# Optimization experiments

Measured on AMD Instinct MI355X. Metric: run time of the kernel, lower is better.

## Reference

```python
import jax, jax.numpy as jnp
import numpy as np

N = 10000
E = 320000
D_IN = 256
D_H = 256
D_OUT = 64
NEG_SLOPE = 0.2


def _segment_softmax(scores, seg, num_segments):
    # numerically stable softmax over variable-size neighborhoods
    m = jax.ops.segment_max(scores, seg, num_segments=num_segments)
    e = jnp.exp(scores - m[seg])
    s = jax.ops.segment_sum(e, seg, num_segments=num_segments)
    return e / s[seg]


def _gatv2_conv(x, src, dst, Wl, bl, Wr, br, att, bias):
    # PyG GATv2Conv, heads=1: lin_l on source, lin_r on target
    xl = x @ Wl + bl              # [N, C]
    xr = x @ Wr + br              # [N, C]
    xj = xl[src]                  # [E, C] source messages
    e = jax.nn.leaky_relu(xj + xr[dst], NEG_SLOPE)   # [E, C]
    score = e @ att               # [E]
    alpha = _segment_softmax(score, dst, N)          # [E]
    out = jax.ops.segment_sum(alpha[:, None] * xj, dst, num_segments=N)
    return out + bias


def setup_inputs() -> dict:
    key = jax.random.key(0)
    ks = jax.random.split(key, 16)
    s1 = 1.0 / np.sqrt(D_IN)
    s2 = 1.0 / np.sqrt(D_H)
    x = jax.random.normal(ks[0], (N, D_IN), dtype=jnp.float32)
    edge_index = jax.random.randint(ks[1], (2, E), 0, N, dtype=jnp.int64)
    return {
        "x": x,
        "W1l": jax.random.normal(ks[2], (D_IN, D_H), jnp.float32) * s1,
        "b1l": jnp.zeros((D_H,), jnp.float32),
        "W1r": jax.random.normal(ks[3], (D_IN, D_H), jnp.float32) * s1,
        "b1r": jnp.zeros((D_H,), jnp.float32),
        "att1": jax.random.normal(ks[4], (D_H,), jnp.float32) * s2,
        "bias1": jnp.zeros((D_H,), jnp.float32),
        "W2l": jax.random.normal(ks[5], (D_H, D_H), jnp.float32) * s2,
        "b2l": jnp.zeros((D_H,), jnp.float32),
        "W2r": jax.random.normal(ks[6], (D_H, D_H), jnp.float32) * s2,
        "b2r": jnp.zeros((D_H,), jnp.float32),
        "att2": jax.random.normal(ks[7], (D_H,), jnp.float32) * s2,
        "bias2": jnp.zeros((D_H,), jnp.float32),
        "Wout": jax.random.normal(ks[8], (D_H, D_OUT), jnp.float32) * s2,
        "bout": jnp.zeros((D_OUT,), jnp.float32),
        "edge_index": edge_index,
    }


def reference(x, W1l, b1l, W1r, b1r, att1, bias1,
              W2l, b2l, W2r, b2r, att2, bias2,
              Wout, bout, edge_index):
    # add self loops (PyG GATv2Conv default)
    loops = jnp.arange(N, dtype=edge_index.dtype)
    src = jnp.concatenate([edge_index[0], loops])
    dst = jnp.concatenate([edge_index[1], loops])

    h = _gatv2_conv(x, src, dst, W1l, b1l, W1r, b1r, att1, bias1)
    h = jax.nn.relu(h)            # norm=Identity, dropout inactive (eval)
    h = _gatv2_conv(h, src, dst, W2l, b2l, W2r, b2r, att2, bias2)
    h = jax.nn.relu(h)
    logits = h @ Wout + bout      # [N, D_OUT]
    return jax.nn.log_softmax(logits, axis=1)
```

## Files before the change

### kernel.cpp

```cpp
#include <hip/hip_runtime.h>
#include <hip/hip_bf16.h>
#include <math.h>

#define N_NODES 10000
#define N_EDGES 320000
#define TOT_E (N_EDGES + N_NODES)
#define D 256
#define DOUT 64
#define NEG_SLOPE 0.2f
#define MAXDEG 128

typedef __attribute__((ext_vector_type(8))) short bf16x8;
typedef __attribute__((ext_vector_type(4))) float f32x4;
typedef unsigned short ushort_t;

__device__ __forceinline__ unsigned short f2b_rne(float f) {
    unsigned int x = __float_as_uint(f);
    x += 0x7FFFu + ((x >> 16) & 1u);
    return (unsigned short)(x >> 16);
}
__device__ __forceinline__ float b2f(unsigned short h) {
    return __uint_as_float(((unsigned int)h) << 16);
}
__device__ __forceinline__ void bsplit(float v, unsigned short& hi, unsigned short& lo) {
    hi = f2b_rne(v);
    lo = f2b_rne(v - b2f(hi));
}

__device__ __forceinline__ void gload16(const ushort_t* g, ushort_t* l) {
    __builtin_amdgcn_global_load_lds(
        (const __attribute__((address_space(1))) void*)g,
        (__attribute__((address_space(3))) void*)l, 16, 0, 0);
}

__device__ __forceinline__ bool detect_f32(const void* x) {
    const ushort_t* xb = (const ushort_t*)x;
    int lane = threadIdx.x & 63;
    int bad = 0;
    #pragma unroll
    for (int i = 0; i < 4; ++i) {
        float v = b2f(xb[2 * (lane + 64 * i)]);
        bad += !(fabsf(v) < 1e4f) ? 1 : 0;
    }
    #pragma unroll
    for (int o = 32; o > 0; o >>= 1) bad += __shfl_down(bad, o);
    return __shfl(bad, 0) > 8;
}
__device__ __forceinline__ bool detect_i64(const int* e32) {
    int lane = threadIdx.x & 63;
    int nz = (e32[2 * lane + 1] != 0) ? 1 : 0;
    #pragma unroll
    for (int o = 32; o > 0; o >>= 1) nz += __shfl_down(nz, o);
    return __shfl(nz, 0) == 0;
}

__global__ __launch_bounds__(256) void prep_kernel(
        const void* x, ushort_t* xh, ushort_t* xlo,
        const void* W1l, const void* W1r, const void* W2l, const void* W2r, const void* Wo,
        const void* v0, const void* v1, const void* v2, const void* v3,
        const void* v4, const void* v5, const void* v6, const void* v7, const void* v8,
        ushort_t* wt, float* vecf, int* counts) {
    bool f32s = detect_f32(x);
    int bid = blockIdx.x;
    int t = threadIdx.x;
    if (bid < 2500) {
        int i = bid * 1024 + t * 4;
        float v[4];
        if (f32s) {
            float4 f = *(const float4*)((const float*)x + i);
            v[0] = f.x; v[1] = f.y; v[2] = f.z; v[3] = f.w;
        } else {
            union { uint2 q; ushort_t u[4]; } r;
            r.q = *(const uint2*)((const ushort_t*)x + i);
            #pragma unroll
            for (int j = 0; j < 4; ++j) v[j] = b2f(r.u[j]);
        }
        union { uint2 q; ushort_t u[4]; } H, L;
        #pragma unroll
        for (int j = 0; j < 4; ++j) bsplit(v[j], H.u[j], L.u[j]);
        *(uint2*)(xh + i) = H.q;
        *(uint2*)(xlo + i) = L.q;
    } else if (bid < 3588) {
        int b = bid - 2500;
        const void* srcs5[5] = {W1l, W1r, W2l, W2r, Wo};
        int wid, n, ncols;
        if (b < 1024) { wid = b >> 8; n = b & 255; ncols = 256; }
        else          { wid = 4;      n = b - 1024; ncols = 64; }
        ushort_t* dh;
        ushort_t* dl;
        if (wid < 4) { dh = wt + (size_t)wid * 2 * 65536; dl = dh + 65536; }
        else         { dh = wt + (size_t)8 * 65536;       dl = dh + 16384; }
        float v = f32s ? ((const float*)srcs5[wid])[(size_t)t * ncols + n]
                       : b2f(((const ushort_t*)srcs5[wid])[(size_t)t * ncols + n]);
        unsigned short hi, lo;
        bsplit(v, hi, lo);
        dh[(size_t)n * 256 + t] = hi;
        dl[(size_t)n * 256 + t] = lo;
    } else if (bid < 3597) {
        int b = bid - 3588;
        const void* ps[9] = {v0, v1, v2, v3, v4, v5, v6, v7, v8};
        int n = (b == 8) ? DOUT : 256;
        if (t < n) {
            float v = f32s ? ((const float*)ps[b])[t] : b2f(((const ushort_t*)ps[b])[t]);
            vecf[b * 256 + t] = v;
        }
    } else {
        int idx = (bid - 3597) * 256 + t;
        if (idx < N_NODES) counts[idx] = 0;
    }
}

__device__ __forceinline__ int eload(const int* ei, bool is64, int idx) {
    int v = is64 ? ei[2 * (size_t)idx] : ei[idx];
    return ((unsigned)v < (unsigned)N_NODES) ? v : 0;
}

__global__ __launch_bounds__(256, 3) void gemm_mfma_kernel(
        const ushort_t* __restrict__ Ahg, const ushort_t* __restrict__ Alg,
        const ushort_t* __restrict__ Wh0, const ushort_t* __restrict__ Wl0,
        const float* __restrict__ bias0, ushort_t* __restrict__ out0,
        const ushort_t* __restrict__ Wh1, const ushort_t* __restrict__ Wl1,
        const float* __restrict__ bias1, ushort_t* __restrict__ out1,
        const int* __restrict__ ei, int* __restrict__ counts,
        int* __restrict__ srcs_pad) {
    __shared__ __align__(16) ushort_t AhL[2][4096];
    __shared__ __align__(16) ushort_t AlL[2][4096];
    __shared__ __align__(16) ushort_t BhL[2][2048];
    __shared__ __align__(16) ushort_t BlL[2][2048];
    int tid = threadIdx.x;
    int lane = tid & 63, wave = tid >> 6;

    if (blockIdx.y >= 79) {
        bool is64 = detect_i64(ei);
        int id = ((blockIdx.y - 79) * 8 + blockIdx.x) * 256 + tid;
        if (id < TOT_E) {
            int src, dst;
            if (id < N_EDGES) { src = eload(ei, is64, id); dst = eload(ei, is64, N_EDGES + id); }
            else              { src = dst = id - N_EDGES; }
            int slot = atomicAdd(&counts[dst], 1);
            if (slot < MAXDEG) srcs_pad[dst * MAXDEG + slot] = src;
        }
        return;
    }

    int lin = blockIdx.x + 8 * blockIdx.y;
    int v = (lin & 7) * 79 + (lin >> 3);
    int row0 = (v >> 3) * 128;
    int y = v & 7;
    const ushort_t* Wh; const ushort_t* Wl; const float* bias;
    ushort_t* outp;
    int col0;
    if (y < 4) { Wh = Wh0; Wl = Wl0; bias = bias0; col0 = y * 64; outp = out0; }
    else       { Wh = Wh1; Wl = Wl1; bias = bias1; col0 = (y - 4) * 64; outp = out1; }

    const ushort_t* gp[6];
    ushort_t* lp0[6];
    ushort_t* lp1[6];
    {
        int lane4 = lane >> 2;
        int qsl = (lane & 3) ^ (lane4 & 3);
        #pragma unroll
        for (int j = 0; j < 6; ++j) {
            int q = wave * 6 + j;
            if (q < 8) {
                gp[j] = Ahg + (size_t)(row0 + q * 16 + lane4) * 256 + qsl * 8;
                lp0[j] = &AhL[0][q * 512]; lp1[j] = &AhL[1][q * 512];
            } else if (q < 16) {
                int r = q - 8;
                gp[j] = Alg + (size_t)(row0 + r * 16 + lane4) * 256 + qsl * 8;
                lp0[j] = &AlL[0][r * 512]; lp1[j] = &AlL[1][r * 512];
            } else if (q < 20) {
                int r = q - 16;
                gp[j] = Wh + (size_t)(col0 + r * 16 + lane4) * 256 + qsl * 8;
                lp0[j] = &BhL[0][r * 512]; lp1[j] = &BhL[1][r * 512];
            } else {
                int r = q - 20;
                gp[j] = Wl + (size_t)(col0 + r * 16 + lane4) * 256 + qsl * 8;
                lp0[j] = &BlL[0][r * 512]; lp1[j] = &BlL[1][r * 512];
            }
        }
    }
    int wm = wave >> 1, wn = wave & 1;
    int l15 = lane & 15;
    int slot = (lane >> 4) ^ (lane & 3);

    f32x4 acc[4][2];
    #pragma unroll
    for (int mg = 0; mg < 4; ++mg)
        #pragma unroll
        for (int ng = 0; ng < 2; ++ng) acc[mg][ng] = (f32x4){0.f, 0.f, 0.f, 0.f};

    #pragma unroll
    for (int j = 0; j < 6; ++j) { gload16(gp[j], lp0[j]); gp[j] += 32; }
    __syncthreads();

    #pragma unroll
    for (int s = 0; s < 8; ++s) {
        const int cb = s & 1;
        if (s < 7) {
            #pragma unroll
            for (int j = 0; j < 6; ++j) {
                gload16(gp[j], cb ? lp0[j] : lp1[j]);
                gp[j] += 32;
            }
        }
        bf16x8 ah[4], al[4];
        #pragma unroll
        for (int mg = 0; mg < 4; ++mg) {
            int o = (wm * 64 + mg * 16 + l15) * 32 + slot * 8;
            ah[mg] = *(const bf16x8*)&AhL[cb][o];
            al[mg] = *(const bf16x8*)&AlL[cb][o];
        }
        #pragma unroll
        for (int ng = 0; ng < 2; ++ng) {
            int o = (wn * 32 + ng * 16 + l15) * 32 + slot * 8;
            bf16x8 b_h = *(const bf16x8*)&BhL[cb][o];
            bf16x8 b_l = *(const bf16x8*)&BlL[cb][o];
            #pragma unroll
            for (int mg = 0; mg < 4; ++mg) {
                acc[mg][ng] = __builtin_amdgcn_mfma_f32_16x16x32_bf16(ah[mg], b_l, acc[mg][ng], 0, 0, 0);
                acc[mg][ng] = __builtin_amdgcn_mfma_f32_16x16x32_bf16(al[mg], b_h, acc[mg][ng], 0, 0, 0);
                acc[mg][ng] = __builtin_amdgcn_mfma_f32_16x16x32_bf16(ah[mg], b_h, acc[mg][ng], 0, 0, 0);
            }
        }
        __syncthreads();
    }

    int quad = lane >> 4;
    #pragma unroll
    for (int ng = 0; ng < 2; ++ng) {
        int col = col0 + wn * 32 + ng * 16 + l15;
        float bv = bias[col];
        #pragma unroll
        for (int mg = 0; mg < 4; ++mg) {
            #pragma unroll
            for (int i = 0; i < 4; ++i) {
                int row = row0 + wm * 64 + mg * 16 + quad * 4 + i;
                if (row < N_NODES) {
                    float vv = acc[mg][ng][i] + bv;
                    outp[(size_t)row * D + col] = f2b_rne(vv);
                }
            }
        }
    }
}

__global__ __launch_bounds__(256) void conv_kernel(const ushort_t* __restrict__ xl,
                                                   const ushort_t* __restrict__ xrb,
                                                   const float* __restrict__ att,
                                                   const float* __restrict__ bias,
                                                   const int* __restrict__ counts,
                                                   const int* __restrict__ srcs_pad,
                                                   ushort_t* __restrict__ hh,
                                                   ushort_t* __restrict__ hl) {
    __shared__ float fbuf[8][256];
    __shared__ float sred[8];
    int node = blockIdx.x;
    int t = threadIdx.x;
    int lane = t & 63;
    int hw = t >> 5;
    int seg = t & 31;
    int deg = counts[node];
    if (deg > MAXDEG) deg = MAXDEG;
    if (deg <= 0) {
        float o = fmaxf(bias[t], 0.f);
        unsigned short hi, lo; bsplit(o, hi, lo);
        hh[(size_t)node * D + t] = hi;
        hl[(size_t)node * D + t] = lo;
        return;
    }
    int s0 = srcs_pad[node * MAXDEG + lane];
    int s1 = srcs_pad[node * MAXDEG + 64 + lane];
    float xr8[8], att8[8];
    {
        union { uint4 q; ushort_t u[8]; } rr;
        rr.q = *(const uint4*)(xrb + (size_t)node * D + seg * 8);
        float4 a0 = *(const float4*)(att + seg * 8);
        float4 a1 = *(const float4*)(att + seg * 8 + 4);
        #pragma unroll
        for (int j = 0; j < 8; ++j) xr8[j] = b2f(rr.u[j]);
        att8[0] = a0.x; att8[1] = a0.y; att8[2] = a0.z; att8[3] = a0.w;
        att8[4] = a1.x; att8[5] = a1.y; att8[6] = a1.z; att8[7] = a1.w;
    }
    float acc8[8];
    #pragma unroll
    for (int j = 0; j < 8; ++j) acc8[j] = 0.f;
    float s = 0.f;

    for (int e0 = 0; e0 < deg; e0 += 32) {
        int dlim = deg - e0; if (dlim > 32) dlim = 32;
        int ni = (dlim > hw) ? ((dlim - hw + 7) >> 3) : 0;
        union { uint4 q; ushort_t u[8]; } r[4];
        #pragma unroll
        for (int i = 0; i < 4; ++i) {
            if (i < ni) {
                int e = e0 + hw + 8 * i;
                int src = __shfl((e < 64) ? s0 : s1, e & 63);
                r[i].q = *(const uint4*)(xl + (size_t)src * D + seg * 8);
            }
        }
        #pragma unroll
        for (int i = 0; i < 4; ++i) {
            if (i < ni) {
                float xf[8];
                #pragma unroll
                for (int j = 0; j < 8; ++j) xf[j] = b2f(r[i].u[j]);
                float p = 0.f;
                #pragma unroll
                for (int j = 0; j < 8; ++j) {
                    float v = xf[j] + xr8[j];
                    v = fmaxf(v, NEG_SLOPE * v);
                    p = fmaf(v, att8[j], p);
                }
                #pragma unroll
                for (int o = 16; o > 0; o >>= 1) p += __shfl_xor(p, o, 32);
                p = __expf(fminf(fmaxf(p, -80.f), 80.f));
                s += p;
                #pragma unroll
                for (int j = 0; j < 8; ++j) acc8[j] = fmaf(p, xf[j], acc8[j]);
            }
        }
    }
    *(float4*)&fbuf[hw][seg * 8] = (float4){acc8[0], acc8[1], acc8[2], acc8[3]};
    *(float4*)&fbuf[hw][seg * 8 + 4] = (float4){acc8[4], acc8[5], acc8[6], acc8[7]};
    if (seg == 0) sred[hw] = s;
    __syncthreads();
    float tot = 0.f;
    #pragma unroll
    for (int k = 0; k < 8; ++k) tot += fbuf[k][t];
    float stot = sred[0];
    #pragma unroll
    for (int k = 1; k < 8; ++k) stot += sred[k];
    float o = tot / stot + bias[t];
    if (!isfinite(o)) o = 0.f;
    o = fmaxf(o, 0.f);
    unsigned short hi, lo; bsplit(o, hi, lo);
    hh[(size_t)node * D + t] = hi;
    hl[(size_t)node * D + t] = lo;
}

__global__ __launch_bounds__(256) void logits_kernel(
        const ushort_t* __restrict__ Ahg, const ushort_t* __restrict__ Alg,
        const ushort_t* __restrict__ Wh, const ushort_t* __restrict__ Wl,
        const float* __restrict__ bias, float* __restrict__ out) {
    __shared__ bf16x8 Ah[4][64];
    __shared__ bf16x8 Al[4][64];
    __shared__ bf16x8 Bh[4][64];
    __shared__ bf16x8 Bl[4][64];
    __shared__ float Cs[64][65];
    __shared__ float mxs[64], lss[64];
    int tid = threadIdx.x;
    int lane = tid & 63, wave = tid >> 6;
    int row0 = blockIdx.x * 64;
    int sm = tid >> 2, skq = tid & 3;
    int sl = skq * 16 + (sm & 15), sr = sm >> 4;

    f32x4 acc[4];
    #pragma unroll
    for (int c = 0; c < 4; ++c) acc[c] = (f32x4){0.f, 0.f, 0.f, 0.f};

    for (int k0 = 0; k0 < D; k0 += 32) {
        uint4 qah, qal;
        int grow = row0 + sm;
        if (grow < N_NODES) {
            size_t aoff = (size_t)grow * D + k0 + skq * 8;
            qah = *(const uint4*)(Ahg + aoff);
            qal = *(const uint4*)(Alg + aoff);
        } else {
            qah = (uint4){0, 0, 0, 0}; qal = (uint4){0, 0, 0, 0};
        }
        size_t boff = (size_t)sm * 256 + k0 + skq * 8;
        uint4 qbh = *(const uint4*)(Wh + boff);
        uint4 qbl = *(const uint4*)(Wl + boff);
        __syncthreads();
        *(uint4*)&Ah[sr][sl] = qah;
        *(uint4*)&Al[sr][sl] = qal;
        *(uint4*)&Bh[sr][sl] = qbh;
        *(uint4*)&Bl[sr][sl] = qbl;
        __syncthreads();
        bf16x8 a_h = Ah[wave][lane];
        bf16x8 a_l = Al[wave][lane];
        #pragma unroll
        for (int c = 0; c < 4; ++c) {
            bf16x8 b_h = Bh[c][lane];
            bf16x8 b_l = Bl[c][lane];
            acc[c] = __builtin_amdgcn_mfma_f32_16x16x32_bf16(a_h, b_l, acc[c], 0, 0, 0);
            acc[c] = __builtin_amdgcn_mfma_f32_16x16x32_bf16(a_l, b_h, acc[c], 0, 0, 0);
            acc[c] = __builtin_amdgcn_mfma_f32_16x16x32_bf16(a_h, b_h, acc[c], 0, 0, 0);
        }
    }
    int quad = lane >> 4;
    #pragma unroll
    for (int c = 0; c < 4; ++c) {
        int col = c * 16 + (lane & 15);
        float bv = bias[col];
        #pragma unroll
        for (int i = 0; i < 4; ++i) {
            int row = wave * 16 + quad * 4 + i;
            Cs[row][col] = acc[c][i] + bv;
        }
    }
    __syncthreads();
    if (tid < 64) {
        float mx = -INFINITY;
        for (int c2 = 0; c2 < 64; ++c2) {
            float v = Cs[tid][c2];
            if (!isfinite(v)) { v = -1e30f; Cs[tid][c2] = v; }
            mx = fmaxf(mx, v);
        }
        float ssum = 0.f;
        for (int c2 = 0; c2 < 64; ++c2) ssum += expf(Cs[tid][c2] - mx);
        mxs[tid] = mx;
        lss[tid] = logf(ssum);
    }
    __syncthreads();
    for (int idx = tid; idx < 64 * 64; idx += 256) {
        int r = idx >> 6, col = idx & 63;
        int grow = row0 + r;
        if (grow < N_NODES) out[(size_t)grow * DOUT + col] = Cs[r][col] - mxs[r] - lss[r];
    }
}

extern "C" void kernel_launch(void* const* d_in, const int* in_sizes, int n_in,
                              void* d_out, int out_size, void* d_ws, size_t ws_size,
                              hipStream_t stream) {
    const void* x    = d_in[0];
    const void* W1l  = d_in[1];
    const void* b1l  = d_in[2];
    const void* W1r  = d_in[3];
    const void* b1r  = d_in[4];
    const void* att1 = d_in[5];
    const void* bia1 = d_in[6];
    const void* W2l  = d_in[7];
    const void* b2l  = d_in[8];
    const void* W2r  = d_in[9];
    const void* b2r  = d_in[10];
    const void* att2 = d_in[11];
    const void* bia2 = d_in[12];
    const void* Wout = d_in[13];
    const void* bout = d_in[14];
    const int*  ei   = (const int*)d_in[15];

    int* counts   = (int*)d_ws;
    int* srcs_pad = counts + N_NODES;
    ushort_t* wt = (ushort_t*)(srcs_pad + (size_t)N_NODES * MAXDEG);
    ushort_t* W1lH = wt;                ushort_t* W1lL = W1lH + 65536;
    ushort_t* W1rH = W1lL + 65536;      ushort_t* W1rL = W1rH + 65536;
    ushort_t* W2lH = W1rL + 65536;      ushort_t* W2lL = W2lH + 65536;
    ushort_t* W2rH = W2lL + 65536;      ushort_t* W2rL = W2rH + 65536;
    ushort_t* WoH  = W2rL + 65536;      ushort_t* WoL  = WoH + 16384;
    float* vecf = (float*)(WoL + 16384);
    ushort_t* xh  = (ushort_t*)(vecf + 9 * 256);
    ushort_t* xlo = xh + (size_t)N_NODES * D;
    ushort_t* xlb = xlo + (size_t)N_NODES * D;
    ushort_t* xrb = xlb + (size_t)N_NODES * D;
    ushort_t* hh = xh;
    ushort_t* hl = xlo;

    float* b1lf = vecf + 0 * 256;
    float* b1rf = vecf + 1 * 256;
    float* att1f = vecf + 2 * 256;
    float* bia1f = vecf + 3 * 256;
    float* b2lf = vecf + 4 * 256;
    float* b2rf = vecf + 5 * 256;
    float* att2f = vecf + 6 * 256;
    float* bia2f = vecf + 7 * 256;
    float* boutf = vecf + 8 * 256;

    prep_kernel<<<3637, 256, 0, stream>>>(x, xh, xlo,
                                          W1l, W1r, W2l, W2r, Wout,
                                          b1l, b1r, att1, bia1, b2l, b2r, att2, bia2, bout,
                                          wt, vecf, counts);

    gemm_mfma_kernel<<<dim3(8, 79 + 162), 256, 0, stream>>>(
        xh, xlo, W1lH, W1lL, b1lf, xlb, W1rH, W1rL, b1rf, xrb,
        ei, counts, srcs_pad);
    conv_kernel<<<N_NODES, 256, 0, stream>>>(xlb, xrb, att1f, bia1f,
                                             counts, srcs_pad, hh, hl);
    gemm_mfma_kernel<<<dim3(8, 79), 256, 0, stream>>>(
        hh, hl, W2lH, W2lL, b2lf, xlb, W2rH, W2rL, b2rf, xrb,
        nullptr, nullptr, nullptr);
    conv_kernel<<<N_NODES, 256, 0, stream>>>(xlb, xrb, att2f, bia2f,
                                             counts, srcs_pad, hh, hl);
    logits_kernel<<<(N_NODES + 63) / 64, 256, 0, stream>>>(hh, hl, WoH, WoL, boutf, (float*)d_out);
}
```

Before: 218.7 us.

## Fuse all stages into one persistent cooperative kernel with grid syncs

Replaces the six separate launches (prep, two GEMMs, two conv passes, logits) with one persistent cooperative mega-kernel. Blocks loop over virtual block indices in each phase, and grid.sync barriers with thread fences sit between phases. This removes launch overhead and inter-kernel gaps, but the grid is capped at occupancy times 256 blocks (at most 768), so each phase runs fewer concurrent blocks. It also adds grid-wide barrier costs and may lower occupancy because of the larger shared memory footprint.

Result: slower. 818.8 us (+274.3%).

```diff
diff --git a/kernel.cpp b/kernel.cpp
--- a/kernel.cpp
+++ b/kernel.cpp
@@ -1,6 +1,9 @@
 #include <hip/hip_runtime.h>
+#include <hip/hip_cooperative_groups.h>
 #include <hip/hip_bf16.h>
 #include <math.h>
+
+namespace cg = cooperative_groups;
 
 #define N_NODES 10000
 #define N_EDGES 320000
@@ -53,97 +56,37 @@
     for (int o = 32; o > 0; o >>= 1) nz += __shfl_down(nz, o);
     return __shfl(nz, 0) == 0;
 }
-
-__global__ __launch_bounds__(256) void prep_kernel(
-        const void* x, ushort_t* xh, ushort_t* xlo,
-        const void* W1l, const void* W1r, const void* W2l, const void* W2r, const void* Wo,
-        const void* v0, const void* v1, const void* v2, const void* v3,
-        const void* v4, const void* v5, const void* v6, const void* v7, const void* v8,
-        ushort_t* wt, float* vecf, int* counts) {
-    bool f32s = detect_f32(x);
-    int bid = blockIdx.x;
-    int t = threadIdx.x;
-    if (bid < 2500) {
-        int i = bid * 1024 + t * 4;
-        float v[4];
-        if (f32s) {
-            float4 f = *(const float4*)((const float*)x + i);
-            v[0] = f.x; v[1] = f.y; v[2] = f.z; v[3] = f.w;
-        } else {
-            union { uint2 q; ushort_t u[4]; } r;
-            r.q = *(const uint2*)((const ushort_t*)x + i);
-            #pragma unroll
-            for (int j = 0; j < 4; ++j) v[j] = b2f(r.u[j]);
-        }
-        union { uint2 q; ushort_t u[4]; } H, L;
-        #pragma unroll
-        for (int j = 0; j < 4; ++j) bsplit(v[j], H.u[j], L.u[j]);
-        *(uint2*)(xh + i) = H.q;
-        *(uint2*)(xlo + i) = L.q;
-    } else if (bid < 3588) {
-        int b = bid - 2500;
-        const void* srcs5[5] = {W1l, W1r, W2l, W2r, Wo};
-        int wid, n, ncols;
-        if (b < 1024) { wid = b >> 8; n = b & 255; ncols = 256; }
-        else          { wid = 4;      n = b - 1024; ncols = 64; }
-        ushort_t* dh;
-        ushort_t* dl;
-        if (wid < 4) { dh = wt + (size_t)wid * 2 * 65536; dl = dh + 65536; }
-        else         { dh = wt + (size_t)8 * 65536;       dl = dh + 16384; }
-        float v = f32s ? ((const float*)srcs5[wid])[(size_t)t * ncols + n]
-                       : b2f(((const ushort_t*)srcs5[wid])[(size_t)t * ncols + n]);
-        unsigned short hi, lo;
-        bsplit(v, hi, lo);
-        dh[(size_t)n * 256 + t] = hi;
-        dl[(size_t)n * 256 + t] = lo;
-    } else if (bid < 3597) {
-        int b = bid - 3588;
-        const void* ps[9] = {v0, v1, v2, v3, v4, v5, v6, v7, v8};
-        int n = (b == 8) ? DOUT : 256;
-        if (t < n) {
-            float v = f32s ? ((const float*)ps[b])[t] : b2f(((const ushort_t*)ps[b])[t]);
-            vecf[b * 256 + t] = v;
-        }
-    } else {
-        int idx = (bid - 3597) * 256 + t;
-        if (idx < N_NODES) counts[idx] = 0;
-    }
-}
-
 __device__ __forceinline__ int eload(const int* ei, bool is64, int idx) {
     int v = is64 ? ei[2 * (size_t)idx] : ei[idx];
     return ((unsigned)v < (unsigned)N_NODES) ? v : 0;
 }
 
-__global__ __launch_bounds__(256, 3) void gemm_mfma_kernel(
-        const ushort_t* __restrict__ Ahg, const ushort_t* __restrict__ Alg,
-        const ushort_t* __restrict__ Wh0, const ushort_t* __restrict__ Wl0,
-        const float* __restrict__ bias0, ushort_t* __restrict__ out0,
-        const ushort_t* __restrict__ Wh1, const ushort_t* __restrict__ Wl1,
-        const float* __restrict__ bias1, ushort_t* __restrict__ out1,
-        const int* __restrict__ ei, int* __restrict__ counts,
-        int* __restrict__ srcs_pad) {
-    __shared__ __align__(16) ushort_t AhL[2][4096];
-    __shared__ __align__(16) ushort_t AlL[2][4096];
-    __shared__ __align__(16) ushort_t BhL[2][2048];
-    __shared__ __align__(16) ushort_t BlL[2][2048];
+struct MegaP {
+    const void* x;
+    const void* W1l; const void* b1l; const void* W1r; const void* b1r;
+    const void* att1; const void* bia1;
+    const void* W2l; const void* b2l; const void* W2r; const void* b2r;
+    const void* att2; const void* bia2;
+    const void* Wout; const void* bout;
+    const int* ei;
+    int* counts; int* srcs_pad;
+    ushort_t* wt; float* vecf;
+    ushort_t* xh; ushort_t* xlo; ushort_t* xlb; ushort_t* xrb;
+    float* out;
+};
+
+__device__ void gemm_tile(unsigned char* SM, int lin,
+                          const ushort_t* Ahg, const ushort_t* Alg,
+                          const ushort_t* Wh0, const ushort_t* Wl0,
+                          const float* bias0, ushort_t* out0,
+                          const ushort_t* Wh1, const ushort_t* Wl1,
+                          const float* bias1, ushort_t* out1) {
+    ushort_t* AhL = (ushort_t*)SM;
+    ushort_t* AlL = AhL + 8192;
+    ushort_t* BhL = AlL + 8192;
+    ushort_t* BlL = BhL + 4096;
     int tid = threadIdx.x;
     int lane = tid & 63, wave = tid >> 6;
-
-    if (blockIdx.y >= 79) {
-        bool is64 = detect_i64(ei);
-        int id = ((blockIdx.y - 79) * 8 + blockIdx.x) * 256 + tid;
-        if (id < TOT_E) {
-            int src, dst;
-            if (id < N_EDGES) { src = eload(ei, is64, id); dst = eload(ei, is64, N_EDGES + id); }
-            else              { src = dst = id - N_EDGES; }
-            int slot = atomicAdd(&counts[dst], 1);
-            if (slot < MAXDEG) srcs_pad[dst * MAXDEG + slot] = src;
-        }
-        return;
-    }
-
-    int lin = blockIdx.x + 8 * blockIdx.y;
     int v = (lin & 7) * 79 + (lin >> 3);
     int row0 = (v >> 3) * 128;
     int y = v & 7;
@@ -164,19 +107,19 @@
             int q = wave * 6 + j;
             if (q < 8) {
                 gp[j] = Ahg + (size_t)(row0 + q * 16 + lane4) * 256 + qsl * 8;
-                lp0[j] = &AhL[0][q * 512]; lp1[j] = &AhL[1][q * 512];
+                lp0[j] = AhL + q * 512; lp1[j] = AhL + 4096 + q * 512;
             } else if (q < 16) {
                 int r = q - 8;
                 gp[j] = Alg + (size_t)(row0 + r * 16 + lane4) * 256 + qsl * 8;
-                lp0[j] = &AlL[0][r * 512]; lp1[j] = &AlL[1][r * 512];
+                lp0[j] = AlL + r * 512; lp1[j] = AlL + 4096 + r * 512;
             } else if (q < 20) {
                 int r = q - 16;
                 gp[j] = Wh + (size_t)(col0 + r * 16 + lane4) * 256 + qsl * 8;
-                lp0[j] = &BhL[0][r * 512]; lp1[j] = &BhL[1][r * 512];
+                lp0[j] = BhL + r * 512; lp1[j] = BhL + 2048 + r * 512;
             } else {
                 int r = q - 20;
                 gp[j] = Wl + (size_t)(col0 + r * 16 + lane4) * 256 + qsl * 8;
-                lp0[j] = &BlL[0][r * 512]; lp1[j] = &BlL[1][r * 512];
+                lp0[j] = BlL + r * 512; lp1[j] = BlL + 2048 + r * 512;
             }
         }
     }
@@ -208,14 +151,14 @@
         #pragma unroll
         for (int mg = 0; mg < 4; ++mg) {
             int o = (wm * 64 + mg * 16 + l15) * 32 + slot * 8;
-            ah[mg] = *(const bf16x8*)&AhL[cb][o];
-            al[mg] = *(const bf16x8*)&AlL[cb][o];
+            ah[mg] = *(const bf16x8*)&AhL[cb * 4096 + o];
+            al[mg] = *(const bf16x8*)&AlL[cb * 4096 + o];
         }
         #pragma unroll
         for (int ng = 0; ng < 2; ++ng) {
             int o = (wn * 32 + ng * 16 + l15) * 32 + slot * 8;
-            bf16x8 b_h = *(const bf16x8*)&BhL[cb][o];
-            bf16x8 b_l = *(const bf16x8*)&BlL[cb][o];
+            bf16x8 b_h = *(const bf16x8*)&BhL[cb * 2048 + o];
+            bf16x8 b_l = *(const bf16x8*)&BlL[cb * 2048 + o];
             #pragma unroll
             for (int mg = 0; mg < 4; ++mg) {
                 acc[mg][ng] = __builtin_amdgcn_mfma_f32_16x16x32_bf16(ah[mg], b_l, acc[mg][ng], 0, 0, 0);
@@ -245,242 +188,330 @@
     }
 }
 
-__global__ __launch_bounds__(256) void conv_kernel(const ushort_t* __restrict__ xl,
-                                                   const ushort_t* __restrict__ xrb,
-                                                   const float* __restrict__ att,
-                                                   const float* __restrict__ bias,
-                                                   const int* __restrict__ counts,
-                                                   const int* __restrict__ srcs_pad,
-                                                   ushort_t* __restrict__ hh,
-                                                   ushort_t* __restrict__ hl) {
-    __shared__ float fbuf[8][256];
-    __shared__ float sred[8];
-    int node = blockIdx.x;
-    int t = threadIdx.x;
-    int lane = t & 63;
-    int hw = t >> 5;
-    int seg = t & 31;
-    int deg = counts[node];
-    if (deg > MAXDEG) deg = MAXDEG;
-    if (deg <= 0) {
-        float o = fmaxf(bias[t], 0.f);
-        unsigned short hi, lo; bsplit(o, hi, lo);
-        hh[(size_t)node * D + t] = hi;
-        hl[(size_t)node * D + t] = lo;
-        return;
-    }
-    int s0 = srcs_pad[node * MAXDEG + lane];
-    int s1 = srcs_pad[node * MAXDEG + 64 + lane];
-    float xr8[8], att8[8];
-    {
-        union { uint4 q; ushort_t u[8]; } rr;
-        rr.q = *(const uint4*)(xrb + (size_t)node * D + seg * 8);
-        float4 a0 = *(const float4*)(att + seg * 8);
-        float4 a1 = *(const float4*)(att + seg * 8 + 4);
-        #pragma unroll
-        for (int j = 0; j < 8; ++j) xr8[j] = b2f(rr.u[j]);
-        att8[0] = a0.x; att8[1] = a0.y; att8[2] = a0.z; att8[3] = a0.w;
-        att8[4] = a1.x; att8[5] = a1.y; att8[6] = a1.z; att8[7] = a1.w;
-    }
-    float acc8[8];
-    #pragma unroll
-    for (int j = 0; j < 8; ++j) acc8[j] = 0.f;
-    float s = 0.f;
-
-    for (int e0 = 0; e0 < deg; e0 += 32) {
-        int dlim = deg - e0; if (dlim > 32) dlim = 32;
-        int ni = (dlim > hw) ? ((dlim - hw + 7) >> 3) : 0;
-        union { uint4 q; ushort_t u[8]; } r[4];
-        #pragma unroll
-        for (int i = 0; i < 4; ++i) {
-            if (i < ni) {
-                int e = e0 + hw + 8 * i;
-                int src = __shfl((e < 64) ? s0 : s1, e & 63);
-                r[i].q = *(const uint4*)(xl + (size_t)src * D + seg * 8);
-            }
-        }
-        #pragma unroll
-        for (int i = 0; i < 4; ++i) {
-            if (i < ni) {
-                float xf[8];
-                #pragma unroll
-                for (int j = 0; j < 8; ++j) xf[j] = b2f(r[i].u[j]);
-                float p = 0.f;
-                #pragma unroll
-                for (int j = 0; j < 8; ++j) {
-                    float v = xf[j] + xr8[j];
-                    v = fmaxf(v, NEG_SLOPE * v);
-                    p = fmaf(v, att8[j], p);
-                }
-                #pragma unroll
-                for (int o = 16; o > 0; o >>= 1) p += __shfl_xor(p, o, 32);
-                p = __expf(fminf(fmaxf(p, -80.f), 80.f));
-                s += p;
-                #pragma unroll
-                for (int j = 0; j < 8; ++j) acc8[j] = fmaf(p, xf[j], acc8[j]);
-            }
-        }
-    }
-    *(float4*)&fbuf[hw][seg * 8] = (float4){acc8[0], acc8[1], acc8[2], acc8[3]};
-    *(float4*)&fbuf[hw][seg * 8 + 4] = (float4){acc8[4], acc8[5], acc8[6], acc8[7]};
-    if (seg == 0) sred[hw] = s;
-    __syncthreads();
-    float tot = 0.f;
-    #pragma unroll
-    for (int k = 0; k < 8; ++k) tot += fbuf[k][t];
-    float stot = sred[0];
-    #pragma unroll
-    for (int k = 1; k < 8; ++k) stot += sred[k];
-    float o = tot / stot + bias[t];
-    if (!isfinite(o)) o = 0.f;
-    o = fmaxf(o, 0.f);
-    unsigned short hi, lo; bsplit(o, hi, lo);
-    hh[(size_t)node * D + t] = hi;
-    hl[(size_t)node * D + t] = lo;
-}
-
-__global__ __launch_bounds__(256) void logits_kernel(
-        const ushort_t* __restrict__ Ahg, const ushort_t* __restrict__ Alg,
-        const ushort_t* __restrict__ Wh, const ushort_t* __restrict__ Wl,
-        const float* __restrict__ bias, float* __restrict__ out) {
-    __shared__ bf16x8 Ah[4][64];
-    __shared__ bf16x8 Al[4][64];
-    __shared__ bf16x8 Bh[4][64];
-    __shared__ bf16x8 Bl[4][64];
-    __shared__ float Cs[64][65];
-    __shared__ float mxs[64], lss[64];
-    int tid = threadIdx.x;
-    int lane = tid & 63, wave = tid >> 6;
-    int row0 = blockIdx.x * 64;
-    int sm = tid >> 2, skq = tid & 3;
-    int sl = skq * 16 + (sm & 15), sr = sm >> 4;
-
-    f32x4 acc[4];
-    #pragma unroll
-    for (int c = 0; c < 4; ++c) acc[c] = (f32x4){0.f, 0.f, 0.f, 0.f};
-
-    for (int k0 = 0; k0 < D; k0 += 32) {
-        uint4 qah, qal;
-        int grow = row0 + sm;
-        if (grow < N_NODES) {
-            size_t aoff = (size_t)grow * D + k0 + skq * 8;
-            qah = *(const uint4*)(Ahg + aoff);
-            qal = *(const uint4*)(Alg + aoff);
-        } else {
-            qah = (uint4){0, 0, 0, 0}; qal = (uint4){0, 0, 0, 0};
-        }
-        size_t boff = (size_t)sm * 256 + k0 + skq * 8;
-        uint4 qbh = *(const uint4*)(Wh + boff);
-        uint4 qbl = *(const uint4*)(Wl + boff);
-        __syncthreads();
-        *(uint4*)&Ah[sr][sl] = qah;
-        *(uint4*)&Al[sr][sl] = qal;
-        *(uint4*)&Bh[sr][sl] = qbh;
-        *(uint4*)&Bl[sr][sl] = qbl;
-        __syncthreads();
-        bf16x8 a_h = Ah[wave][lane];
-        bf16x8 a_l = Al[wave][lane];
-        #pragma unroll
-        for (int c = 0; c < 4; ++c) {
-            bf16x8 b_h = Bh[c][lane];
-            bf16x8 b_l = Bl[c][lane];
-            acc[c] = __builtin_amdgcn_mfma_f32_16x16x32_bf16(a_h, b_l, acc[c], 0, 0, 0);
-            acc[c] = __builtin_amdgcn_mfma_f32_16x16x32_bf16(a_l, b_h, acc[c], 0, 0, 0);
-            acc[c] = __builtin_amdgcn_mfma_f32_16x16x32_bf16(a_h, b_h, acc[c], 0, 0, 0);
-        }
-    }
-    int quad = lane >> 4;
-    #pragma unroll
-    for (int c = 0; c < 4; ++c) {
-        int col = c * 16 + (lane & 15);
-        float bv = bias[col];
-        #pragma unroll
-        for (int i = 0; i < 4; ++i) {
-            int row = wave * 16 + quad * 4 + i;
-            Cs[row][col] = acc[c][i] + bv;
-        }
-    }
-    __syncthreads();
-    if (tid < 64) {
-        float mx = -INFINITY;
-        for (int c2 = 0; c2 < 64; ++c2) {
-            float v = Cs[tid][c2];
-            if (!isfinite(v)) { v = -1e30f; Cs[tid][c2] = v; }
-            mx = fmaxf(mx, v);
-        }
-        float ssum = 0.f;
-        for (int c2 = 0; c2 < 64; ++c2) ssum += expf(Cs[tid][c2] - mx);
-        mxs[tid] = mx;
-        lss[tid] = logf(ssum);
-    }
-    __syncthreads();
-    for (int idx = tid; idx < 64 * 64; idx += 256) {
-        int r = idx >> 6, col = idx & 63;
-        int grow = row0 + r;
-        if (grow < N_NODES) out[(size_t)grow * DOUT + col] = Cs[r][col] - mxs[r] - lss[r];
-    }
-}
-
-extern "C" void kernel_launch(void* const* d_in, const int* in_sizes, int n_in,
-                              void* d_out, int out_size, void* d_ws, size_t ws_size,
-                              hipStream_t stream) {
-    const void* x    = d_in[0];
-    const void* W1l  = d_in[1];
-    const void* b1l  = d_in[2];
-    const void* W1r  = d_in[3];
-    const void* b1r  = d_in[4];
-    const void* att1 = d_in[5];
-    const void* bia1 = d_in[6];
-    const void* W2l  = d_in[7];
-    const void* b2l  = d_in[8];
-    const void* W2r  = d_in[9];
-    const void* b2r  = d_in[10];
-    const void* att2 = d_in[11];
-    const void* bia2 = d_in[12];
-    const void* Wout = d_in[13];
-    const void* bout = d_in[14];
-    const int*  ei   = (const int*)d_in[15];
-
-    int* counts   = (int*)d_ws;
-    int* srcs_pad = counts + N_NODES;
-    ushort_t* wt = (ushort_t*)(srcs_pad + (size_t)N_NODES * MAXDEG);
-    ushort_t* W1lH = wt;                ushort_t* W1lL = W1lH + 65536;
+__global__ __launch_bounds__(256, 3) void mega_kernel(MegaP P) {
+    cg::grid_group grid = cg::this_grid();
+    __shared__ __align__(16) unsigned char SM[49152];
+    const int nb = gridDim.x;
+    const int bid0 = blockIdx.x;
+    const int t = threadIdx.x;
+    const int lane = t & 63;
+
+    ushort_t* W1lH = P.wt;              ushort_t* W1lL = W1lH + 65536;
     ushort_t* W1rH = W1lL + 65536;      ushort_t* W1rL = W1rH + 65536;
     ushort_t* W2lH = W1rL + 65536;      ushort_t* W2lL = W2lH + 65536;
     ushort_t* W2rH = W2lL + 65536;      ushort_t* W2rL = W2rH + 65536;
     ushort_t* WoH  = W2rL + 65536;      ushort_t* WoL  = WoH + 16384;
-    float* vecf = (float*)(WoL + 16384);
+    float* b1lf = P.vecf + 0 * 256;
+    float* b1rf = P.vecf + 1 * 256;
+    float* att1f = P.vecf + 2 * 256;
+    float* bia1f = P.vecf + 3 * 256;
+    float* b2lf = P.vecf + 4 * 256;
+    float* b2rf = P.vecf + 5 * 256;
+    float* att2f = P.vecf + 6 * 256;
+    float* bia2f = P.vecf + 7 * 256;
+    float* boutf = P.vecf + 8 * 256;
+    ushort_t* hh = P.xh;
+    ushort_t* hl = P.xlo;
+
+    {
+        bool f32s = detect_f32(P.x);
+        for (int bid = bid0; bid < 3637; bid += nb) {
+            if (bid < 2500) {
+                int i = bid * 1024 + t * 4;
+                float v[4];
+                if (f32s) {
+                    float4 f = *(const float4*)((const float*)P.x + i);
+                    v[0] = f.x; v[1] = f.y; v[2] = f.z; v[3] = f.w;
+                } else {
+                    union { uint2 q; ushort_t u[4]; } r;
+                    r.q = *(const uint2*)((const ushort_t*)P.x + i);
+                    #pragma unroll
+                    for (int j = 0; j < 4; ++j) v[j] = b2f(r.u[j]);
+                }
+                union { uint2 q; ushort_t u[4]; } H, L;
+                #pragma unroll
+                for (int j = 0; j < 4; ++j) bsplit(v[j], H.u[j], L.u[j]);
+                *(uint2*)(P.xh + i) = H.q;
+                *(uint2*)(P.xlo + i) = L.q;
+            } else if (bid < 3588) {
+                int b = bid - 2500;
+                const void* srcs5[5] = {P.W1l, P.W1r, P.W2l, P.W2r, P.Wout};
+                int wid, n, ncols;
+                if (b < 1024) { wid = b >> 8; n = b & 255; ncols = 256; }
+                else          { wid = 4;      n = b - 1024; ncols = 64; }
+                ushort_t* dh;
+                ushort_t* dl;
+                if (wid < 4) { dh = P.wt + (size_t)wid * 2 * 65536; dl = dh + 65536; }
+                else         { dh = P.wt + (size_t)8 * 65536;       dl = dh + 16384; }
+                float v = f32s ? ((const float*)srcs5[wid])[(size_t)t * ncols + n]
+                               : b2f(((const ushort_t*)srcs5[wid])[(size_t)t * ncols + n]);
+                unsigned short hi, lo;
+                bsplit(v, hi, lo);
+                dh[(size_t)n * 256 + t] = hi;
+                dl[(size_t)n * 256 + t] = lo;
+            } else if (bid < 3597) {
+                int b = bid - 3588;
+                const void* ps[9] = {P.b1l, P.b1r, P.att1, P.bia1,
+                                     P.b2l, P.b2r, P.att2, P.bia2, P.bout};
+                int n = (b == 8) ? DOUT : 256;
+                if (t < n) {
+                    float v = f32s ? ((const float*)ps[b])[t]
+                                   : b2f(((const ushort_t*)ps[b])[t]);
+                    P.vecf[b * 256 + t] = v;
+                }
+            } else {
+                int idx = (bid - 3597) * 256 + t;
+                if (idx < N_NODES) P.counts[idx] = 0;
+            }
+        }
+    }
+    __threadfence();
+    grid.sync();
+    __threadfence();
+
+    {
+        bool is64 = detect_i64(P.ei);
+        for (int u = bid0; u < 632 + 1290; u += nb) {
+            if (u < 632) {
+                gemm_tile(SM, u, P.xh, P.xlo, W1lH, W1lL, b1lf, P.xlb,
+                          W1rH, W1rL, b1rf, P.xrb);
+            } else {
+                int id = (u - 632) * 256 + t;
+                if (id < TOT_E) {
+                    int src, dst;
+                    if (id < N_EDGES) { src = eload(P.ei, is64, id); dst = eload(P.ei, is64, N_EDGES + id); }
+                    else              { src = dst = id - N_EDGES; }
+                    int slot = atomicAdd(&P.counts[dst], 1);
+                    if (slot < MAXDEG) P.srcs_pad[dst * MAXDEG + slot] = src;
+                }
+            }
+        }
+    }
+    __threadfence();
+    grid.sync();
+    __threadfence();
+
+    for (int layer = 0; layer < 2; ++layer) {
+        {
+            const ushort_t* xl = P.xlb;
+            const ushort_t* xrb = P.xrb;
+            const float* att = layer ? att2f : att1f;
+            const float* bias = layer ? bia2f : bia1f;
+            float* fbuf = (float*)SM;
+            float* sred = (float*)(SM + 8192);
+            int hw = t >> 5, seg = t & 31;
+            for (int node = bid0; node < N_NODES; node += nb) {
+                int deg = P.counts[node];
+                if (deg > MAXDEG) deg = MAXDEG;
+                if (deg <= 0) {
+                    float o = fmaxf(bias[t], 0.f);
+                    unsigned short hi, lo; bsplit(o, hi, lo);
+                    hh[(size_t)node * D + t] = hi;
+                    hl[(size_t)node * D + t] = lo;
+                    continue;
+                }
+                int s0 = P.srcs_pad[node * MAXDEG + lane];
+                int s1 = P.srcs_pad[node * MAXDEG + 64 + lane];
+                float xr8[8], att8[8];
+                {
+                    union { uint4 q; ushort_t u[8]; } rr;
+                    rr.q = *(const uint4*)(xrb + (size_t)node * D + seg * 8);
+                    float4 a0 = *(const float4*)(att + seg * 8);
+                    float4 a1 = *(const float4*)(att + seg * 8 + 4);
+                    #pragma unroll
+                    for (int j = 0; j < 8; ++j) xr8[j] = b2f(rr.u[j]);
+                    att8[0] = a0.x; att8[1] = a0.y; att8[2] = a0.z; att8[3] = a0.w;
+                    att8[4] = a1.x; att8[5] = a1.y; att8[6] = a1.z; att8[7] = a1.w;
+                }
+                float acc8[8];
+                #pragma unroll
+                for (int j = 0; j < 8; ++j) acc8[j] = 0.f;
+                float s = 0.f;
+                for (int e0 = 0; e0 < deg; e0 += 32) {
+                    int dlim = deg - e0; if (dlim > 32) dlim = 32;
+                    int ni = (dlim > hw) ? ((dlim - hw + 7) >> 3) : 0;
+                    union { uint4 q; ushort_t u[8]; } r[4];
+                    #pragma unroll
+                    for (int i = 0; i < 4; ++i) {
+                        if (i < ni) {
+                            int e = e0 + hw + 8 * i;
+                            int src = __shfl((e < 64) ? s0 : s1, e & 63);
+                            r[i].q = *(const uint4*)(xl + (size_t)src * D + seg * 8);
+                        }
+                    }
+                    #pragma unroll
+                    for (int i = 0; i < 4; ++i) {
+                        if (i < ni) {
+                            float xf[8];
+                            #pragma unroll
+                            for (int j = 0; j < 8; ++j) xf[j] = b2f(r[i].u[j]);
+                            float p = 0.f;
+                            #pragma unroll
+                            for (int j = 0; j < 8; ++j) {
+                                float v = xf[j] + xr8[j];
+                                v = fmaxf(v, NEG_SLOPE * v);
+                                p = fmaf(v, att8[j], p);
+                            }
+                            #pragma unroll
+                            for (int o = 16; o > 0; o >>= 1) p += __shfl_xor(p, o, 32);
+                            p = __expf(fminf(fmaxf(p, -80.f), 80.f));
+                            s += p;
+                            #pragma unroll
+                            for (int j = 0; j < 8; ++j) acc8[j] = fmaf(p, xf[j], acc8[j]);
+                        }
+                    }
+                }
+                __syncthreads();
+                *(float4*)&fbuf[hw * 256 + seg * 8] = (float4){acc8[0], acc8[1], acc8[2], acc8[3]};
+                *(float4*)&fbuf[hw * 256 + seg * 8 + 4] = (float4){acc8[4], acc8[5], acc8[6], acc8[7]};
+                if (seg == 0) sred[hw] = s;
+                __syncthreads();
+                float tot = 0.f;
+                #pragma unroll
+                for (int k = 0; k < 8; ++k) tot += fbuf[k * 256 + t];
+                float stot = sred[0];
+                #pragma unroll
+                for (int k = 1; k < 8; ++k) stot += sred[k];
+                float o = tot / stot + bias[t];
+                if (!isfinite(o)) o = 0.f;
+                o = fmaxf(o, 0.f);
+                unsigned short hi, lo; bsplit(o, hi, lo);
+                hh[(size_t)node * D + t] = hi;
+                hl[(size_t)node * D + t] = lo;
+            }
+        }
+        __threadfence();
+        grid.sync();
+        __threadfence();
+
+        if (layer == 0) {
+            for (int u = bid0; u < 632; u += nb) {
+                gemm_tile(SM, u, hh, hl, W2lH, W2lL, b2lf, P.xlb,
+                          W2rH, W2rL, b2rf, P.xrb);
+            }
+            __threadfence();
+            grid.sync();
+            __threadfence();
+        }
+    }
+
+    {
+        bf16x8* Ah = (bf16x8*)SM;
+        bf16x8* Al = Ah + 256;
+        bf16x8* Bh = Al + 256;
+        bf16x8* Bl = Bh + 256;
+        float* Cs = (float*)(SM + 16384);
+        float* mxs = (float*)(SM + 16384 + 16640);
+        float* lss = mxs + 64;
+        int tid = t;
+        int wave = tid >> 6;
+        int sm_ = tid >> 2, skq = tid & 3;
+        int sl = skq * 16 + (sm_ & 15), sr = sm_ >> 4;
+        for (int u = bid0; u < (N_NODES + 63) / 64; u += nb) {
+            int row0 = u * 64;
+            f32x4 acc[4];
+            #pragma unroll
+            for (int c = 0; c < 4; ++c) acc[c] = (f32x4){0.f, 0.f, 0.f, 0.f};
+            for (int k0 = 0; k0 < D; k0 += 32) {
+                uint4 qah, qal;
+                int grow = row0 + sm_;
+                if (grow < N_NODES) {
+                    size_t aoff = (size_t)grow * D + k0 + skq * 8;
+                    qah = *(const uint4*)(hh + aoff);
+                    qal = *(const uint4*)(hl + aoff);
+                } else {
+                    qah = (uint4){0, 0, 0, 0}; qal = (uint4){0, 0, 0, 0};
+                }
+                size_t boff = (size_t)sm_ * 256 + k0 + skq * 8;
+                uint4 qbh = *(const uint4*)(WoH + boff);
+                uint4 qbl = *(const uint4*)(WoL + boff);
+                __syncthreads();
+                *(uint4*)&Ah[sr * 64 + sl] = qah;
+                *(uint4*)&Al[sr * 64 + sl] = qal;
+                *(uint4*)&Bh[sr * 64 + sl] = qbh;
+                *(uint4*)&Bl[sr * 64 + sl] = qbl;
+                __syncthreads();
+                bf16x8 a_h = Ah[wave * 64 + lane];
+                bf16x8 a_l = Al[wave * 64 + lane];
+                #pragma unroll
+                for (int c = 0; c < 4; ++c) {
+                    bf16x8 b_h = Bh[c * 64 + lane];
+                    bf16x8 b_l = Bl[c * 64 + lane];
+                    acc[c] = __builtin_amdgcn_mfma_f32_16x16x32_bf16(a_h, b_l, acc[c], 0, 0, 0);
+                    acc[c] = __builtin_amdgcn_mfma_f32_16x16x32_bf16(a_l, b_h, acc[c], 0, 0, 0);
+                    acc[c] = __builtin_amdgcn_mfma_f32_16x16x32_bf16(a_h, b_h, acc[c], 0, 0, 0);
+                }
+            }
+            int quad = lane >> 4;
+            __syncthreads();
+            #pragma unroll
+            for (int c = 0; c < 4; ++c) {
+                int col = c * 16 + (lane & 15);
+                float bv = boutf[col];
+                #pragma unroll
+                for (int i = 0; i < 4; ++i) {
+                    int row = wave * 16 + quad * 4 + i;
+                    Cs[row * 65 + col] = acc[c][i] + bv;
+                }
+            }
+            __syncthreads();
+            if (tid < 64) {
+                float mx = -INFINITY;
+                for (int c2 = 0; c2 < 64; ++c2) {
+                    float v = Cs[tid * 65 + c2];
+                    if (!isfinite(v)) { v = -1e30f; Cs[tid * 65 + c2] = v; }
+                    mx = fmaxf(mx, v);
+                }
+                float ssum = 0.f;
+                for (int c2 = 0; c2 < 64; ++c2) ssum += expf(Cs[tid * 65 + c2] - mx);
+                mxs[tid] = mx;
+                lss[tid] = logf(ssum);
+            }
+            __syncthreads();
+            for (int idx = tid; idx < 64 * 64; idx += 256) {
+                int r = idx >> 6, col = idx & 63;
+                int grow = row0 + r;
+                if (grow < N_NODES)
+                    P.out[(size_t)grow * DOUT + col] = Cs[r * 65 + col] - mxs[r] - lss[r];
+            }
+            __syncthreads();
+        }
+    }
+}
+
+extern "C" void kernel_launch(void* const* d_in, const int* in_sizes, int n_in,
+                              void* d_out, int out_size, void* d_ws, size_t ws_size,
+                              hipStream_t stream) {
+    int* counts   = (int*)d_ws;
+    int* srcs_pad = counts + N_NODES;
+    ushort_t* wt = (ushort_t*)(srcs_pad + (size_t)N_NODES * MAXDEG);
+    float* vecf = (float*)(wt + 8 * 65536 + 2 * 16384);
     ushort_t* xh  = (ushort_t*)(vecf + 9 * 256);
     ushort_t* xlo = xh + (size_t)N_NODES * D;
     ushort_t* xlb = xlo + (size_t)N_NODES * D;
     ushort_t* xrb = xlb + (size_t)N_NODES * D;
-    ushort_t* hh = xh;
-    ushort_t* hl = xlo;
-
-    float* b1lf = vecf + 0 * 256;
-    float* b1rf = vecf + 1 * 256;
-    float* att1f = vecf + 2 * 256;
-    float* bia1f = vecf + 3 * 256;
-    float* b2lf = vecf + 4 * 256;
-    float* b2rf = vecf + 5 * 256;
-    float* att2f = vecf + 6 * 256;
-    float* bia2f = vecf + 7 * 256;
-    float* boutf = vecf + 8 * 256;
-
-    prep_kernel<<<3637, 256, 0, stream>>>(x, xh, xlo,
-                                          W1l, W1r, W2l, W2r, Wout,
-                                          b1l, b1r, att1, bia1, b2l, b2r, att2, bia2, bout,
-                                          wt, vecf, counts);
-
-    gemm_mfma_kernel<<<dim3(8, 79 + 162), 256, 0, stream>>>(
-        xh, xlo, W1lH, W1lL, b1lf, xlb, W1rH, W1rL, b1rf, xrb,
-        ei, counts, srcs_pad);
-    conv_kernel<<<N_NODES, 256, 0, stream>>>(xlb, xrb, att1f, bia1f,
-                                             counts, srcs_pad, hh, hl);
-    gemm_mfma_kernel<<<dim3(8, 79), 256, 0, stream>>>(
-        hh, hl, W2lH, W2lL, b2lf, xlb, W2rH, W2rL, b2rf, xrb,
-        nullptr, nullptr, nullptr);
-    conv_kernel<<<N_NODES, 256, 0, stream>>>(xlb, xrb, att2f, bia2f,
-                                             counts, srcs_pad, hh, hl);
-    logits_kernel<<<(N_NODES + 63) / 64, 256, 0, stream>>>(hh, hl, WoH, WoL, boutf, (float*)d_out);
-}
+
+    MegaP P;
+    P.x = d_in[0];
+    P.W1l = d_in[1];  P.b1l = d_in[2];  P.W1r = d_in[3];  P.b1r = d_in[4];
+    P.att1 = d_in[5]; P.bia1 = d_in[6];
+    P.W2l = d_in[7];  P.b2l = d_in[8];  P.W2r = d_in[9];  P.b2r = d_in[10];
+    P.att2 = d_in[11]; P.bia2 = d_in[12];
+    P.Wout = d_in[13]; P.bout = d_in[14];
+    P.ei = (const int*)d_in[15];
+    P.counts = counts; P.srcs_pad = srcs_pad;
+    P.wt = wt; P.vecf = vecf;
+    P.xh = xh; P.xlo = xlo; P.xlb = xlb; P.xrb = xrb;
+    P.out = (float*)d_out;
+
+    static int s_grid = 0;
+    if (s_grid == 0) {
+        int mb = 0;
+        hipOccupancyMaxActiveBlocksPerMultiprocessor(&mb, mega_kernel, 256, 0);
+        if (mb < 1) mb = 1;
+        s_grid = mb * 256;
+        if (s_grid > 768) s_grid = 768;
+    }
+    void* kargs[] = { (void*)&P };
+    hipLaunchCooperativeKernel(mega_kernel, dim3(s_grid), dim3(256), kargs, 0, stream);
+}
```
